# Kernel optimization log

Hardware: AMD Instinct MI355X
Metric: run time of the kernel (lower is better)

## Reference

```python
import jax, jax.numpy as jnp
import numpy as np

B, S, D = 16, 1024, 1024

def _xavier_uniform(key, shape, fan_in, fan_out):
    a = float(np.sqrt(6.0 / (fan_in + fan_out)))
    return jax.random.uniform(key, shape, jnp.float32, -a, a)

def setup_inputs() -> dict:
    key = jax.random.key(0)
    ks = jax.random.split(key, 8)
    query = jax.random.normal(ks[0], (B, S, D), jnp.float32)
    key_t = jax.random.normal(ks[1], (B, S, D), jnp.float32)
    value = jax.random.normal(ks[2], (B, S, D), jnp.float32)
    # learned additive attention bias [1, S, S], xavier_uniform init
    attn_bias = _xavier_uniform(ks[3], (1, S, S), S, S)
    # Linear weights (torch nn.Linear default: kaiming-uniform-ish; any init ok for baseline)
    Wq = _xavier_uniform(ks[4], (D, D), D, D)
    bq = jnp.zeros((D,), jnp.float32)
    Wk = _xavier_uniform(ks[5], (D, D), D, D)
    bk = jnp.zeros((D,), jnp.float32)
    return {"query": query, "key": key_t, "value": value,
            "attn_bias": attn_bias, "Wq": Wq, "bq": bq, "Wk": Wk, "bk": bk}

def reference(query, key, value, attn_bias, Wq, bq, Wk, bk):
    # q = query @ Wq^T + bq  (torch Linear convention)
    q = jnp.einsum('bsd,ed->bse', query, Wq) + bq            # [B,S,D]
    k = jnp.einsum('bsd,ed->bse', key, Wk) + bk              # [B,S,D]
    energy = jnp.einsum('bsd,btd->bst', q, k) + attn_bias    # [B,S,S] (bias broadcasts over B)
    attention = jax.nn.softmax(energy, axis=-1)
    out = jnp.einsum('bst,btd->bsd', attention, value)       # value is NOT projected (matches source)
    return (out, attention)
```

## Files before the change

### kernel.cpp

```cpp
#include <hip/hip_runtime.h>


#define AS1 __attribute__((address_space(1)))
#define AS3 __attribute__((address_space(3)))
#define VMCNT(n) asm volatile("s_waitcnt vmcnt(" #n ")" ::: "memory")
#define LGKM(n)  asm volatile("s_waitcnt lgkmcnt(" #n ")" ::: "memory")
#define SBARRIER asm volatile("s_barrier" ::: "memory")
#define SB0 __builtin_amdgcn_sched_barrier(0)

typedef __bf16 bf16;
typedef __bf16 bf16x4 __attribute__((ext_vector_type(4)));
typedef __bf16 bf16x8 __attribute__((ext_vector_type(8)));
typedef float  f32x4  __attribute__((ext_vector_type(4)));
typedef float  f32x16 __attribute__((ext_vector_type(16)));

constexpr int BATCH = 16;
constexpr int S = 1024;
constexpr int D = 1024;
constexpr long NBSD = (long)BATCH * S * D;

constexpr int GBM = 256, GBN = 256, GBK = 32;
constexpr int NTK = 1024 / GBK;
constexpr int ARR = GBM * GBK;

__device__ __forceinline__ void stage16(const bf16* src, const bf16* dst) {
  __builtin_amdgcn_global_load_lds((const AS1 void*)src, (AS3 void*)dst, 16, 0, 0);
}

__global__ __launch_bounds__(256) void split_convert(
    const float* __restrict__ in, bf16* __restrict__ hi, bf16* __restrict__ lo, int n4) {
  int i = blockIdx.x * blockDim.x + threadIdx.x;
  int stride = gridDim.x * blockDim.x;
  for (; i < n4; i += stride) {
    f32x4 x = ((const f32x4*)in)[i];
    bf16x4 h, l;
#pragma unroll
    for (int j = 0; j < 4; ++j) {
      float v = x[j];
      bf16 hh = (bf16)v;
      h[j] = hh;
      l[j] = (bf16)(v - (float)hh);
    }
    ((bf16x4*)hi)[i] = h;
    ((bf16x4*)lo)[i] = l;
  }
}

__global__ __launch_bounds__(256) void transpose_convert(
    const float* __restrict__ v, bf16* __restrict__ vT) {
  __shared__ float tile[32][33];
  const int b = blockIdx.z;
  const int t0 = blockIdx.y * 32, d0 = blockIdx.x * 32;
  const int tx = threadIdx.x & 31, ty = threadIdx.x >> 5;
  const float* src = v + (long)b * S * D;
#pragma unroll
  for (int i = 0; i < 4; ++i)
    tile[ty + i * 8][tx] = src[(long)(t0 + ty + i * 8) * D + d0 + tx];
  __syncthreads();
  bf16* dst = vT + (long)b * D * S;
#pragma unroll
  for (int i = 0; i < 4; ++i)
    dst[(long)(d0 + ty + i * 8) * S + t0 + tx] = (bf16)tile[tx][ty + i * 8];
}

template <int EPI>
__global__ __launch_bounds__(512, 2) void gemm32_split(
    const bf16* __restrict__ Ah_g, const bf16* __restrict__ Al_g, long a_bs,
    const bf16* __restrict__ Bh_g, const bf16* __restrict__ Bl_g, long b_bs,
    const float* __restrict__ bias,
    bf16* __restrict__ Ch, bf16* __restrict__ Cl,
    float* __restrict__ Cf, long c_bs) {
  __shared__ bf16 lds[2 * 4 * ARR];

  const int tid = threadIdx.x;
  const int lane = tid & 63, wid = tid >> 6;
  const int wr = wid >> 2, wc = wid & 3;
  const int lr = lane & 31;
  const int lk = lane >> 5;

  const int w = blockIdx.x;
  const int swz = (w & 7) * 32 + (w >> 3);
  int z, by, bx;
  if constexpr (EPI == 0) { z = 0; by = swz >> 2; bx = swz & 3; }
  else { z = swz >> 4; by = (swz >> 2) & 3; bx = swz & 3; }
  const long brow = (long)by * GBM, bcol = (long)bx * GBN;

  const bf16* A_h = Ah_g + (long)z * a_bs;
  const bf16* A_l = Al_g + (long)z * a_bs;
  const bf16* B_h = Bh_g + (long)z * b_bs;
  const bf16* B_l = Bl_g + (long)z * b_bs;

  const int srow = tid >> 2;
  const int csw = ((tid & 3) ^ ((srow >> 1) & 3)) * 8;
  const long asrc = (brow + srow) * 1024 + csw;
  const long bsrc = (bcol + srow) * 1024 + csw;
  const int dstoff = wid * 512;

  int aoff[4][2], boff[2][2];
#pragma unroll
  for (int i = 0; i < 4; ++i) {
    const int r = wr * 128 + i * 32 + lr;
#pragma unroll
    for (int s = 0; s < 2; ++s)
      aoff[i][s] = r * 32 + (((2 * s + lk) ^ ((r >> 1) & 3)) * 8);
  }
#pragma unroll
  for (int j = 0; j < 2; ++j) {
    const int r = wc * 64 + j * 32 + lr;
#pragma unroll
    for (int s = 0; s < 2; ++s)
      boff[j][s] = r * 32 + (((2 * s + lk) ^ ((r >> 1) & 3)) * 8);
  }

  f32x16 acc[4][2] = {};
  bf16x8 ahA[4][2], bhA[2][2], ahB[4][2], bhB[2][2], al[4][2], bl[2][2];

#define STG(slot, arr, base, koff, rr) \
  stage16((base) + (koff) + (long)(rr) * 131072, \
          lds + ((slot) * 4 + (arr)) * ARR + (rr) * 4096 + dstoff)

#define CLUSTER(AF, BF) \
  __builtin_amdgcn_s_setprio(1); \
  _Pragma("unroll") \
  for (int s = 0; s < 2; ++s) \
    _Pragma("unroll") \
    for (int i = 0; i < 4; ++i) \
      _Pragma("unroll") \
      for (int j = 0; j < 2; ++j) \
        acc[i][j] = __builtin_amdgcn_mfma_f32_32x32x16_bf16(AF[i][s], BF[j][s], acc[i][j], 0, 0, 0); \
  __builtin_amdgcn_s_setprio(0)

#define TILE_BODY(AH, BH, AHN, BHN, CUR, NXT, PF, KN) \
  { \
    const bf16* lA_l = lds + ((CUR) * 4 + 1) * ARR; \
    const bf16* lB_l = lds + ((CUR) * 4 + 3) * ARR; \
    const bf16* nA_h = lds + ((NXT) * 4 + 0) * ARR; \
    const bf16* nB_h = lds + ((NXT) * 4 + 2) * ARR; \
     \
    if (PF) { \
      STG(NXT, 0, A_h + asrc, KN, 0); STG(NXT, 0, A_h + asrc, KN, 1); \
      STG(NXT, 2, B_h + bsrc, KN, 0); STG(NXT, 2, B_h + bsrc, KN, 1); \
      VMCNT(6); \
    } else { VMCNT(2); } \
    SBARRIER; \
    _Pragma("unroll") \
    for (int j = 0; j < 2; ++j) \
      _Pragma("unroll") \
      for (int s = 0; s < 2; ++s) bl[j][s] = *(const bf16x8*)&lB_l[boff[j][s]]; \
    LGKM(4); SB0; \
    CLUSTER(AH, BH); \
     \
    if (PF) { STG(NXT, 3, B_l + bsrc, KN, 0); STG(NXT, 3, B_l + bsrc, KN, 1); VMCNT(6); } \
    else { VMCNT(0); } \
    SBARRIER; \
    _Pragma("unroll") \
    for (int i = 0; i < 4; ++i) \
      _Pragma("unroll") \
      for (int s = 0; s < 2; ++s) al[i][s] = *(const bf16x8*)&lA_l[aoff[i][s]]; \
    LGKM(8); SB0; \
    CLUSTER(AH, bl); \
     \
    if (PF) { STG(NXT, 1, A_l + asrc, KN, 0); STG(NXT, 1, A_l + asrc, KN, 1); VMCNT(4); } \
    SBARRIER; \
    if (PF) { \
      _Pragma("unroll") \
      for (int i = 0; i < 4; ++i) \
        _Pragma("unroll") \
        for (int s = 0; s < 2; ++s) AHN[i][s] = *(const bf16x8*)&nA_h[aoff[i][s]]; \
      _Pragma("unroll") \
      for (int j = 0; j < 2; ++j) \
        _Pragma("unroll") \
        for (int s = 0; s < 2; ++s) BHN[j][s] = *(const bf16x8*)&nB_h[boff[j][s]]; \
      LGKM(12); \
    } else { LGKM(0); } \
    SB0; \
    CLUSTER(al, BH); \
  }

  STG(0, 0, A_h + asrc, 0, 0); STG(0, 0, A_h + asrc, 0, 1);
  STG(0, 2, B_h + bsrc, 0, 0); STG(0, 2, B_h + bsrc, 0, 1);
  STG(0, 3, B_l + bsrc, 0, 0); STG(0, 3, B_l + bsrc, 0, 1);
  STG(0, 1, A_l + asrc, 0, 0); STG(0, 1, A_l + asrc, 0, 1);
  VMCNT(4);
  SBARRIER;
  {
    const bf16* lA_h0 = lds;
    const bf16* lB_h0 = lds + 2 * ARR;
#pragma unroll
    for (int i = 0; i < 4; ++i)
#pragma unroll
      for (int s = 0; s < 2; ++s) ahA[i][s] = *(const bf16x8*)&lA_h0[aoff[i][s]];
#pragma unroll
    for (int j = 0; j < 2; ++j)
#pragma unroll
      for (int s = 0; s < 2; ++s) bhA[j][s] = *(const bf16x8*)&lB_h0[boff[j][s]];
  }

  for (int tt = 0; tt < 15; ++tt) {
    const long k1 = (long)(2 * tt + 1) * GBK;
    const long k2 = (long)(2 * tt + 2) * GBK;
    TILE_BODY(ahA, bhA, ahB, bhB, 0, 1, true, k1);
    TILE_BODY(ahB, bhB, ahA, bhA, 1, 0, true, k2);
  }
  TILE_BODY(ahA, bhA, ahB, bhB, 0, 1, true, (long)31 * GBK);
  TILE_BODY(ahB, bhB, ahA, bhA, 1, 0, false, 0);
#undef STG
#undef CLUSTER
#undef TILE_BODY

  if constexpr (EPI == 0) {
#pragma unroll
    for (int j = 0; j < 2; ++j) {
      const long col = bcol + wc * 64 + j * 32 + lr;
      const float bv = bias[col];
#pragma unroll
      for (int i = 0; i < 4; ++i) {
        const long row0 = brow + wr * 128 + i * 32 + 4 * lk;
#pragma unroll
        for (int r = 0; r < 16; ++r) {
          const long row = row0 + (r & 3) + 8 * (r >> 2);
          const float c = acc[i][j][r] + bv;
          const bf16 h = (bf16)c;
          const bf16 l = (bf16)(c - (float)h);
          const long idx = row * 1024 + col;
          Ch[idx] = h;
          Cl[idx] = l;
        }
      }
    }
  } else {
    float* Cz = Cf + (long)z * c_bs;
#pragma unroll
    for (int j = 0; j < 2; ++j) {
      const long col = bcol + wc * 64 + j * 32 + lr;
#pragma unroll
      for (int i = 0; i < 4; ++i) {
        const long row0 = brow + wr * 128 + i * 32 + 4 * lk;
#pragma unroll
        for (int r = 0; r < 16; ++r) {
          const long row = row0 + (r & 3) + 8 * (r >> 2);
          Cz[row * 1024 + col] = acc[i][j][r] + bias[row * 1024 + col];
        }
      }
    }
  }
}

__global__ __launch_bounds__(512, 2) void gemm8_plain(
    const bf16* __restrict__ A_g, long a_bs,
    const bf16* __restrict__ B_g, long b_bs,
    float* __restrict__ C, long c_bs) {
  __shared__ bf16 lds[2 * 2 * ARR];

  const int tid = threadIdx.x;
  const int lane = tid & 63, wid = tid >> 6;
  const int wr = wid >> 2, wc = wid & 3;
  const int fr = lane & 15, fq = lane >> 4;
  const int fsw = (fr >> 1) & 3;

  const int w = blockIdx.x;
  const int swz = (w & 7) * 32 + (w >> 3);
  const int z = swz >> 4, by = (swz >> 2) & 3, bx = swz & 3;
  const long brow = (long)by * GBM, bcol = (long)bx * GBN;

  const bf16* A = A_g + (long)z * a_bs;
  const bf16* B = B_g + (long)z * b_bs;

  const int srow = tid >> 2;
  const int csw = ((tid & 3) ^ ((srow >> 1) & 3)) * 8;
  const long asrc = (brow + srow) * 1024 + csw;
  const long bsrc = (bcol + srow) * 1024 + csw;
  const int dstoff = wid * 512;

  const int aoffb = (wr * 128 + fr) * 32 + (fq ^ fsw) * 8;
  const int boffb = (wc * 64 + fr) * 32 + (fq ^ fsw) * 8;

  f32x4 acc[8][4] = {};

#define STG2(slot, arr, base, koff, rr) \
  stage16((base) + (koff) + (long)(rr) * 131072, \
          lds + ((slot) * 2 + (arr)) * ARR + (rr) * 4096 + dstoff)

  STG2(0, 0, A + asrc, 0, 0); STG2(0, 0, A + asrc, 0, 1);
  STG2(0, 1, B + bsrc, 0, 0); STG2(0, 1, B + bsrc, 0, 1);

  for (int t = 0; t < NTK; ++t) {
    const int cur = t & 1, nxt = cur ^ 1;
    const bf16* lA = lds + (cur * 2 + 0) * ARR;
    const bf16* lB = lds + (cur * 2 + 1) * ARR;

    if (t + 1 < NTK) {
      const long kn = (long)(t + 1) * GBK;
      STG2(nxt, 0, A + asrc, kn, 0); STG2(nxt, 0, A + asrc, kn, 1);
      STG2(nxt, 1, B + bsrc, kn, 0); STG2(nxt, 1, B + bsrc, kn, 1);
      VMCNT(4);
    } else {
      VMCNT(0);
    }
    SB0;
    SBARRIER;

    bf16x8 ah[8], bh[4];
#pragma unroll
    for (int m = 0; m < 8; ++m) ah[m] = *(const bf16x8*)&lA[aoffb + m * 512];
#pragma unroll
    for (int n = 0; n < 4; ++n) bh[n] = *(const bf16x8*)&lB[boffb + n * 512];
#pragma unroll
    for (int n = 0; n < 4; ++n)
#pragma unroll
      for (int m = 0; m < 8; ++m)
        acc[m][n] = __builtin_amdgcn_mfma_f32_16x16x32_bf16(ah[m], bh[n], acc[m][n], 0, 0, 0);

    SBARRIER;
  }
#undef STG2

  float* Cz = C + (long)z * c_bs;
#pragma unroll
  for (int n = 0; n < 4; ++n) {
    const long col = bcol + wc * 64 + n * 16 + fr;
#pragma unroll
    for (int m = 0; m < 8; ++m) {
      const long row0 = brow + wr * 128 + m * 16 + fq * 4;
#pragma unroll
      for (int j = 0; j < 4; ++j)
        Cz[(row0 + j) * 1024 + col] = acc[m][n][j];
    }
  }
}

__global__ __launch_bounds__(256) void softmax_rows(
    float* __restrict__ attn, bf16* __restrict__ attn_bf) {
  const long row = blockIdx.x;
  float* p = attn + row * 1024;
  const int tid = threadIdx.x, lane = tid & 63, wid = tid >> 6;

  f32x4 x = ((const f32x4*)p)[tid];
  float m = fmaxf(fmaxf(x[0], x[1]), fmaxf(x[2], x[3]));
#pragma unroll
  for (int off = 32; off; off >>= 1) m = fmaxf(m, __shfl_xor(m, off));
  __shared__ float redm[4];
  if (lane == 0) redm[wid] = m;
  __syncthreads();
  m = fmaxf(fmaxf(redm[0], redm[1]), fmaxf(redm[2], redm[3]));

  f32x4 e;
#pragma unroll
  for (int j = 0; j < 4; ++j) e[j] = __expf(x[j] - m);
  float s = e[0] + e[1] + e[2] + e[3];
#pragma unroll
  for (int off = 32; off; off >>= 1) s += __shfl_xor(s, off);
  __shared__ float reds[4];
  if (lane == 0) reds[wid] = s;
  __syncthreads();
  s = reds[0] + reds[1] + reds[2] + reds[3];

  const float inv = 1.0f / s;
  f32x4 r;
  bf16x4 rb;
#pragma unroll
  for (int j = 0; j < 4; ++j) {
    r[j] = e[j] * inv;
    rb[j] = (bf16)r[j];
  }
  ((f32x4*)p)[tid] = r;
  ((bf16x4*)(attn_bf + row * 1024))[tid] = rb;
}

extern "C" void kernel_launch(void* const* d_in, const int* in_sizes, int n_in,
                              void* d_out, int out_size, void* d_ws, size_t ws_size,
                              hipStream_t stream) {
  const float* query     = (const float*)d_in[0];
  const float* key       = (const float*)d_in[1];
  const float* value     = (const float*)d_in[2];
  const float* attn_bias = (const float*)d_in[3];
  const float* Wq        = (const float*)d_in[4];
  const float* bq        = (const float*)d_in[5];
  const float* Wk        = (const float*)d_in[6];
  const float* bk        = (const float*)d_in[7];

  float* out  = (float*)d_out;
  float* attn = out + NBSD;

  bf16* ws    = (bf16*)d_ws;
  bf16* q_hi  = ws;
  bf16* q_lo  = ws + NBSD;
  bf16* k_hi  = ws + 2 * NBSD;
  bf16* k_lo  = ws + 3 * NBSD;
  bf16* Wq_hi = ws + 4 * NBSD;
  bf16* Wq_lo = Wq_hi + (long)D * D;
  bf16* Wk_hi = Wq_lo + (long)D * D;
  bf16* Wk_lo = Wk_hi + (long)D * D;
  bf16* scr   = Wk_lo + (long)D * D;
  bf16* key_hi = scr;
  bf16* key_lo = scr + NBSD;
  bf16* valueT  = scr;
  bf16* attn_bf = scr + NBSD;
  bf16* query_hi = (bf16*)d_out;
  bf16* query_lo = query_hi + NBSD;

  split_convert<<<2048, 256, 0, stream>>>(query, query_hi, query_lo, (int)(NBSD / 4));
  split_convert<<<2048, 256, 0, stream>>>(key, key_hi, key_lo, (int)(NBSD / 4));
  split_convert<<<512, 256, 0, stream>>>(Wq, Wq_hi, Wq_lo, D * D / 4);
  split_convert<<<512, 256, 0, stream>>>(Wk, Wk_hi, Wk_lo, D * D / 4);

  gemm32_split<0><<<256, 512, 0, stream>>>(query_hi, query_lo, 0, Wq_hi, Wq_lo, 0,
                                           bq, q_hi, q_lo, nullptr, 0);
  gemm32_split<0><<<256, 512, 0, stream>>>(key_hi, key_lo, 0, Wk_hi, Wk_lo, 0,
                                           bk, k_hi, k_lo, nullptr, 0);

  transpose_convert<<<dim3(32, 32, 16), 256, 0, stream>>>(value, valueT);

  gemm32_split<1><<<256, 512, 0, stream>>>(q_hi, q_lo, (long)S * D, k_hi, k_lo, (long)S * D,
                                           attn_bias, nullptr, nullptr, attn, (long)S * S);

  softmax_rows<<<BATCH * S, 256, 0, stream>>>(attn, attn_bf);

  gemm8_plain<<<256, 512, 0, stream>>>(attn_bf, (long)S * S, valueT, (long)D * S,
                                       out, (long)S * D);
}
```

Baseline: 478.1 us.

## Fuse convert and projection launches, simplify split-GEMM pipeline, use 32x32 MFMA

Merges the four split_convert launches into one kernel and the two projection GEMMs into a single 512-block launch, so fewer kernels run back to back and each one fills the GPU better. The split-bf16 K loop drops the hand-interleaved double-register prefetch for a simpler loop that loads fragments and waits on lgkmcnt(0) before each MFMA cluster. This removes LDS/MFMA overlap inside a tile and adds barriers. The final plain GEMM moves from 16x16x32 to 32x32x16 MFMA with the same fragment layout as the split kernels.

```diff
diff --git a/kernel.cpp b/kernel.cpp
--- a/kernel.cpp
+++ b/kernel.cpp
@@ -27,10 +27,11 @@
   __builtin_amdgcn_global_load_lds((const AS1 void*)src, (AS3 void*)dst, 16, 0, 0);
 }
 
-__global__ __launch_bounds__(256) void split_convert(
-    const float* __restrict__ in, bf16* __restrict__ hi, bf16* __restrict__ lo, int n4) {
-  int i = blockIdx.x * blockDim.x + threadIdx.x;
-  int stride = gridDim.x * blockDim.x;
+__device__ __forceinline__ void conv_body(
+    const float* __restrict__ in, bf16* __restrict__ hi, bf16* __restrict__ lo,
+    int n4, int bid, int nb) {
+  int i = bid * 256 + threadIdx.x;
+  const int stride = nb * 256;
   for (; i < n4; i += stride) {
     f32x4 x = ((const f32x4*)in)[i];
     bf16x4 h, l;
@@ -46,6 +47,20 @@
   }
 }
 
+__global__ __launch_bounds__(256) void fused_converts(
+    const float* __restrict__ query, const float* __restrict__ key,
+    const float* __restrict__ Wq, const float* __restrict__ Wk,
+    bf16* __restrict__ q_hi, bf16* __restrict__ q_lo,
+    bf16* __restrict__ k_hi, bf16* __restrict__ k_lo,
+    bf16* __restrict__ Wq_hi, bf16* __restrict__ Wq_lo,
+    bf16* __restrict__ Wk_hi, bf16* __restrict__ Wk_lo) {
+  const int b = blockIdx.x;
+  if (b < 2048)       conv_body(query, q_hi, q_lo, (int)(NBSD / 4), b, 2048);
+  else if (b < 4096)  conv_body(key,  k_hi, k_lo, (int)(NBSD / 4), b - 2048, 2048);
+  else if (b < 4608)  conv_body(Wq, Wq_hi, Wq_lo, D * D / 4, b - 4096, 512);
+  else                conv_body(Wk, Wk_hi, Wk_lo, D * D / 4, b - 4608, 512);
+}
+
 __global__ __launch_bounds__(256) void transpose_convert(
     const float* __restrict__ v, bf16* __restrict__ vT) {
   __shared__ float tile[32][33];
@@ -63,14 +78,201 @@
     dst[(long)(d0 + ty + i * 8) * S + t0 + tx] = (bf16)tile[tx][ty + i * 8];
 }
 
-template <int EPI>
-__global__ __launch_bounds__(512, 2) void gemm32_split(
+#define STGM(slot, arr, base, koff, rr) \
+  stage16((base) + (koff) + (long)(rr) * 131072, \
+          lds + ((slot) * 4 + (arr)) * ARR + (rr) * 4096 + dstoff)
+
+#define CLUSTERM(AF, BF) \
+  __builtin_amdgcn_s_setprio(1); \
+  _Pragma("unroll") \
+  for (int s = 0; s < 2; ++s) \
+    _Pragma("unroll") \
+    for (int i = 0; i < 4; ++i) \
+      _Pragma("unroll") \
+      for (int j = 0; j < 2; ++j) \
+        acc[i][j] = __builtin_amdgcn_mfma_f32_32x32x16_bf16(AF[i][s], BF[j][s], acc[i][j], 0, 0, 0); \
+  __builtin_amdgcn_s_setprio(0)
+
+#define SPLIT_KLOOP \
+  STGM(0, 0, A_h + asrc, 0, 0); STGM(0, 0, A_h + asrc, 0, 1); \
+  STGM(0, 2, B_h + bsrc, 0, 0); STGM(0, 2, B_h + bsrc, 0, 1); \
+  STGM(0, 3, B_l + bsrc, 0, 0); STGM(0, 3, B_l + bsrc, 0, 1); \
+  STGM(0, 1, A_l + asrc, 0, 0); STGM(0, 1, A_l + asrc, 0, 1); \
+  VMCNT(4); \
+  SBARRIER; \
+  for (int t = 0; t < NTK; ++t) { \
+    const int cur = t & 1, nxt = cur ^ 1; \
+    const long kn = (long)(t + 1) * GBK; \
+    const bool pf = (t + 1 < NTK); \
+    const bf16* lA_h = lds + (cur * 4 + 0) * ARR; \
+    const bf16* lA_l = lds + (cur * 4 + 1) * ARR; \
+    const bf16* lB_h = lds + (cur * 4 + 2) * ARR; \
+    const bf16* lB_l = lds + (cur * 4 + 3) * ARR; \
+    _Pragma("unroll") \
+    for (int i = 0; i < 4; ++i) \
+      _Pragma("unroll") \
+      for (int s = 0; s < 2; ++s) ah[i][s] = *(const bf16x8*)&lA_h[aoff[i][s]]; \
+    _Pragma("unroll") \
+    for (int j = 0; j < 2; ++j) \
+      _Pragma("unroll") \
+      for (int s = 0; s < 2; ++s) bh[j][s] = *(const bf16x8*)&lB_h[boff[j][s]]; \
+    if (pf) { \
+      STGM(nxt, 0, A_h + asrc, kn, 0); STGM(nxt, 0, A_h + asrc, kn, 1); \
+      STGM(nxt, 2, B_h + bsrc, kn, 0); STGM(nxt, 2, B_h + bsrc, kn, 1); \
+      VMCNT(6); \
+    } else { VMCNT(2); } \
+    SBARRIER; LGKM(0); SB0; \
+    CLUSTERM(ah, bh); \
+    SBARRIER; \
+    _Pragma("unroll") \
+    for (int j = 0; j < 2; ++j) \
+      _Pragma("unroll") \
+      for (int s = 0; s < 2; ++s) bl[j][s] = *(const bf16x8*)&lB_l[boff[j][s]]; \
+    if (pf) { \
+      STGM(nxt, 3, B_l + bsrc, kn, 0); STGM(nxt, 3, B_l + bsrc, kn, 1); \
+      VMCNT(6); \
+    } else { VMCNT(0); } \
+    SBARRIER; LGKM(0); SB0; \
+    CLUSTERM(ah, bl); \
+    SBARRIER; \
+    _Pragma("unroll") \
+    for (int i = 0; i < 4; ++i) \
+      _Pragma("unroll") \
+      for (int s = 0; s < 2; ++s) al[i][s] = *(const bf16x8*)&lA_l[aoff[i][s]]; \
+    if (pf) { \
+      STGM(nxt, 1, A_l + asrc, kn, 0); STGM(nxt, 1, A_l + asrc, kn, 1); \
+      VMCNT(4); \
+    } \
+    SBARRIER; LGKM(0); SB0; \
+    CLUSTERM(al, bh); \
+    SBARRIER; \
+  }
+
+#define SPLIT_PREAMBLE \
+  const int tid = threadIdx.x; \
+  const int lane = tid & 63, wid = tid >> 6; \
+  const int wr = wid >> 2, wc = wid & 3; \
+  const int lr = lane & 31; \
+  const int lk = lane >> 5; \
+  const int srow = tid >> 2; \
+  const int csw = ((tid & 3) ^ ((srow >> 1) & 3)) * 8; \
+  const int dstoff = wid * 512; \
+  int aoff[4][2], boff[2][2]; \
+  _Pragma("unroll") \
+  for (int i = 0; i < 4; ++i) { \
+    const int r = wr * 128 + i * 32 + lr; \
+    _Pragma("unroll") \
+    for (int s = 0; s < 2; ++s) \
+      aoff[i][s] = r * 32 + (((2 * s + lk) ^ ((r >> 1) & 3)) * 8); \
+  } \
+  _Pragma("unroll") \
+  for (int j = 0; j < 2; ++j) { \
+    const int r = wc * 64 + j * 32 + lr; \
+    _Pragma("unroll") \
+    for (int s = 0; s < 2; ++s) \
+      boff[j][s] = r * 32 + (((2 * s + lk) ^ ((r >> 1) & 3)) * 8); \
+  } \
+  f32x16 acc[4][2] = {}; \
+  bf16x8 ah[4][2], al[4][2], bh[2][2], bl[2][2];
+
+__global__ __launch_bounds__(512, 2) void gemm32_proj2(
+    const bf16* __restrict__ qh, const bf16* __restrict__ ql,
+    const bf16* __restrict__ kh, const bf16* __restrict__ kl,
+    const bf16* __restrict__ Wqh, const bf16* __restrict__ Wql,
+    const bf16* __restrict__ Wkh, const bf16* __restrict__ Wkl,
+    const float* __restrict__ bq, const float* __restrict__ bk,
+    bf16* __restrict__ qoh, bf16* __restrict__ qol,
+    bf16* __restrict__ koh, bf16* __restrict__ kol) {
+  __shared__ bf16 lds[2 * 4 * ARR];
+
+  SPLIT_PREAMBLE
+
+  const int w = blockIdx.x;
+  const int swz = (w & 7) * 64 + (w >> 3);
+  const int op = swz >> 8;
+  const int rem = swz & 255;
+  const int by = rem >> 2, bx = rem & 3;
+  const long brow = (long)by * GBM, bcol = (long)bx * GBN;
+
+  const bf16* A_h = op ? kh : qh;
+  const bf16* A_l = op ? kl : ql;
+  const bf16* B_h = op ? Wkh : Wqh;
+  const bf16* B_l = op ? Wkl : Wql;
+  const float* bias = op ? bk : bq;
+  bf16* Ch = op ? koh : qoh;
+  bf16* Cl = op ? kol : qol;
+
+  const long asrc = (brow + srow) * 1024 + csw;
+  const long bsrc = (bcol + srow) * 1024 + csw;
+
+  SPLIT_KLOOP
+
+#pragma unroll
+  for (int j = 0; j < 2; ++j) {
+    const long col = bcol + wc * 64 + j * 32 + lr;
+    const float bv = bias[col];
+#pragma unroll
+    for (int i = 0; i < 4; ++i) {
+      const long row0 = brow + wr * 128 + i * 32 + 4 * lk;
+#pragma unroll
+      for (int r = 0; r < 16; ++r) {
+        const long row = row0 + (r & 3) + 8 * (r >> 2);
+        const float c = acc[i][j][r] + bv;
+        const bf16 h = (bf16)c;
+        const bf16 l = (bf16)(c - (float)h);
+        const long idx = row * 1024 + col;
+        Ch[idx] = h;
+        Cl[idx] = l;
+      }
+    }
+  }
+}
+
+__global__ __launch_bounds__(512, 2) void gemm32_energy(
     const bf16* __restrict__ Ah_g, const bf16* __restrict__ Al_g, long a_bs,
     const bf16* __restrict__ Bh_g, const bf16* __restrict__ Bl_g, long b_bs,
     const float* __restrict__ bias,
-    bf16* __restrict__ Ch, bf16* __restrict__ Cl,
     float* __restrict__ Cf, long c_bs) {
   __shared__ bf16 lds[2 * 4 * ARR];
+
+  SPLIT_PREAMBLE
+
+  const int w = blockIdx.x;
+  const int swz = (w & 7) * 32 + (w >> 3);
+  const int z = swz >> 4, by = (swz >> 2) & 3, bx = swz & 3;
+  const long brow = (long)by * GBM, bcol = (long)bx * GBN;
+
+  const bf16* A_h = Ah_g + (long)z * a_bs;
+  const bf16* A_l = Al_g + (long)z * a_bs;
+  const bf16* B_h = Bh_g + (long)z * b_bs;
+  const bf16* B_l = Bl_g + (long)z * b_bs;
+
+  const long asrc = (brow + srow) * 1024 + csw;
+  const long bsrc = (bcol + srow) * 1024 + csw;
+
+  SPLIT_KLOOP
+
+  float* Cz = Cf + (long)z * c_bs;
+#pragma unroll
+  for (int j = 0; j < 2; ++j) {
+    const long col = bcol + wc * 64 + j * 32 + lr;
+#pragma unroll
+    for (int i = 0; i < 4; ++i) {
+      const long row0 = brow + wr * 128 + i * 32 + 4 * lk;
+#pragma unroll
+      for (int r = 0; r < 16; ++r) {
+        const long row = row0 + (r & 3) + 8 * (r >> 2);
+        Cz[row * 1024 + col] = acc[i][j][r] + bias[row * 1024 + col];
+      }
+    }
+  }
+}
+
+__global__ __launch_bounds__(512, 2) void gemm32_plain(
+    const bf16* __restrict__ A_g, long a_bs,
+    const bf16* __restrict__ B_g, long b_bs,
+    float* __restrict__ C, long c_bs) {
+  __shared__ bf16 lds[2 * 2 * ARR];
 
   const int tid = threadIdx.x;
   const int lane = tid & 63, wid = tid >> 6;
@@ -80,15 +282,11 @@
 
   const int w = blockIdx.x;
   const int swz = (w & 7) * 32 + (w >> 3);
-  int z, by, bx;
-  if constexpr (EPI == 0) { z = 0; by = swz >> 2; bx = swz & 3; }
-  else { z = swz >> 4; by = (swz >> 2) & 3; bx = swz & 3; }
+  const int z = swz >> 4, by = (swz >> 2) & 3, bx = swz & 3;
   const long brow = (long)by * GBM, bcol = (long)bx * GBN;
 
-  const bf16* A_h = Ah_g + (long)z * a_bs;
-  const bf16* A_l = Al_g + (long)z * a_bs;
-  const bf16* B_h = Bh_g + (long)z * b_bs;
-  const bf16* B_l = Bl_g + (long)z * b_bs;
+  const bf16* A = A_g + (long)z * a_bs;
+  const bf16* B = B_g + (long)z * b_bs;
 
   const int srow = tid >> 2;
   const int csw = ((tid & 3) ^ ((srow >> 1) & 3)) * 8;
@@ -113,169 +311,7 @@
   }
 
   f32x16 acc[4][2] = {};
-  bf16x8 ahA[4][2], bhA[2][2], ahB[4][2], bhB[2][2], al[4][2], bl[2][2];
-
-#define STG(slot, arr, base, koff, rr) \
-  stage16((base) + (koff) + (long)(rr) * 131072, \
-          lds + ((slot) * 4 + (arr)) * ARR + (rr) * 4096 + dstoff)
-
-#define CLUSTER(AF, BF) \
-  __builtin_amdgcn_s_setprio(1); \
-  _Pragma("unroll") \
-  for (int s = 0; s < 2; ++s) \
-    _Pragma("unroll") \
-    for (int i = 0; i < 4; ++i) \
-      _Pragma("unroll") \
-      for (int j = 0; j < 2; ++j) \
-        acc[i][j] = __builtin_amdgcn_mfma_f32_32x32x16_bf16(AF[i][s], BF[j][s], acc[i][j], 0, 0, 0); \
-  __builtin_amdgcn_s_setprio(0)
-
-#define TILE_BODY(AH, BH, AHN, BHN, CUR, NXT, PF, KN) \
-  { \
-    const bf16* lA_l = lds + ((CUR) * 4 + 1) * ARR; \
-    const bf16* lB_l = lds + ((CUR) * 4 + 3) * ARR; \
-    const bf16* nA_h = lds + ((NXT) * 4 + 0) * ARR; \
-    const bf16* nB_h = lds + ((NXT) * 4 + 2) * ARR; \
-     \
-    if (PF) { \
-      STG(NXT, 0, A_h + asrc, KN, 0); STG(NXT, 0, A_h + asrc, KN, 1); \
-      STG(NXT, 2, B_h + bsrc, KN, 0); STG(NXT, 2, B_h + bsrc, KN, 1); \
-      VMCNT(6); \
-    } else { VMCNT(2); } \
-    SBARRIER; \
-    _Pragma("unroll") \
-    for (int j = 0; j < 2; ++j) \
-      _Pragma("unroll") \
-      for (int s = 0; s < 2; ++s) bl[j][s] = *(const bf16x8*)&lB_l[boff[j][s]]; \
-    LGKM(4); SB0; \
-    CLUSTER(AH, BH); \
-     \
-    if (PF) { STG(NXT, 3, B_l + bsrc, KN, 0); STG(NXT, 3, B_l + bsrc, KN, 1); VMCNT(6); } \
-    else { VMCNT(0); } \
-    SBARRIER; \
-    _Pragma("unroll") \
-    for (int i = 0; i < 4; ++i) \
-      _Pragma("unroll") \
-      for (int s = 0; s < 2; ++s) al[i][s] = *(const bf16x8*)&lA_l[aoff[i][s]]; \
-    LGKM(8); SB0; \
-    CLUSTER(AH, bl); \
-     \
-    if (PF) { STG(NXT, 1, A_l + asrc, KN, 0); STG(NXT, 1, A_l + asrc, KN, 1); VMCNT(4); } \
-    SBARRIER; \
-    if (PF) { \
-      _Pragma("unroll") \
-      for (int i = 0; i < 4; ++i) \
-        _Pragma("unroll") \
-        for (int s = 0; s < 2; ++s) AHN[i][s] = *(const bf16x8*)&nA_h[aoff[i][s]]; \
-      _Pragma("unroll") \
-      for (int j = 0; j < 2; ++j) \
-        _Pragma("unroll") \
-        for (int s = 0; s < 2; ++s) BHN[j][s] = *(const bf16x8*)&nB_h[boff[j][s]]; \
-      LGKM(12); \
-    } else { LGKM(0); } \
-    SB0; \
-    CLUSTER(al, BH); \
-  }
-
-  STG(0, 0, A_h + asrc, 0, 0); STG(0, 0, A_h + asrc, 0, 1);
-  STG(0, 2, B_h + bsrc, 0, 0); STG(0, 2, B_h + bsrc, 0, 1);
-  STG(0, 3, B_l + bsrc, 0, 0); STG(0, 3, B_l + bsrc, 0, 1);
-  STG(0, 1, A_l + asrc, 0, 0); STG(0, 1, A_l + asrc, 0, 1);
-  VMCNT(4);
-  SBARRIER;
-  {
-    const bf16* lA_h0 = lds;
-    const bf16* lB_h0 = lds + 2 * ARR;
-#pragma unroll
-    for (int i = 0; i < 4; ++i)
-#pragma unroll
-      for (int s = 0; s < 2; ++s) ahA[i][s] = *(const bf16x8*)&lA_h0[aoff[i][s]];
-#pragma unroll
-    for (int j = 0; j < 2; ++j)
-#pragma unroll
-      for (int s = 0; s < 2; ++s) bhA[j][s] = *(const bf16x8*)&lB_h0[boff[j][s]];
-  }
-
-  for (int tt = 0; tt < 15; ++tt) {
-    const long k1 = (long)(2 * tt + 1) * GBK;
-    const long k2 = (long)(2 * tt + 2) * GBK;
-    TILE_BODY(ahA, bhA, ahB, bhB, 0, 1, true, k1);
-    TILE_BODY(ahB, bhB, ahA, bhA, 1, 0, true, k2);
-  }
-  TILE_BODY(ahA, bhA, ahB, bhB, 0, 1, true, (long)31 * GBK);
-  TILE_BODY(ahB, bhB, ahA, bhA, 1, 0, false, 0);
-#undef STG
-#undef CLUSTER
-#undef TILE_BODY
-
-  if constexpr (EPI == 0) {
-#pragma unroll
-    for (int j = 0; j < 2; ++j) {
-      const long col = bcol + wc * 64 + j * 32 + lr;
-      const float bv = bias[col];
-#pragma unroll
-      for (int i = 0; i < 4; ++i) {
-        const long row0 = brow + wr * 128 + i * 32 + 4 * lk;
-#pragma unroll
-        for (int r = 0; r < 16; ++r) {
-          const long row = row0 + (r & 3) + 8 * (r >> 2);
-          const float c = acc[i][j][r] + bv;
-          const bf16 h = (bf16)c;
-          const bf16 l = (bf16)(c - (float)h);
-          const long idx = row * 1024 + col;
-          Ch[idx] = h;
-          Cl[idx] = l;
-        }
-      }
-    }
-  } else {
-    float* Cz = Cf + (long)z * c_bs;
-#pragma unroll
-    for (int j = 0; j < 2; ++j) {
-      const long col = bcol + wc * 64 + j * 32 + lr;
-#pragma unroll
-      for (int i = 0; i < 4; ++i) {
-        const long row0 = brow + wr * 128 + i * 32 + 4 * lk;
-#pragma unroll
-        for (int r = 0; r < 16; ++r) {
-          const long row = row0 + (r & 3) + 8 * (r >> 2);
-          Cz[row * 1024 + col] = acc[i][j][r] + bias[row * 1024 + col];
-        }
-      }
-    }
-  }
-}
-
-__global__ __launch_bounds__(512, 2) void gemm8_plain(
-    const bf16* __restrict__ A_g, long a_bs,
-    const bf16* __restrict__ B_g, long b_bs,
-    float* __restrict__ C, long c_bs) {
-  __shared__ bf16 lds[2 * 2 * ARR];
-
-  const int tid = threadIdx.x;
-  const int lane = tid & 63, wid = tid >> 6;
-  const int wr = wid >> 2, wc = wid & 3;
-  const int fr = lane & 15, fq = lane >> 4;
-  const int fsw = (fr >> 1) & 3;
-
-  const int w = blockIdx.x;
-  const int swz = (w & 7) * 32 + (w >> 3);
-  const int z = swz >> 4, by = (swz >> 2) & 3, bx = swz & 3;
-  const long brow = (long)by * GBM, bcol = (long)bx * GBN;
-
-  const bf16* A = A_g + (long)z * a_bs;
-  const bf16* B = B_g + (long)z * b_bs;
-
-  const int srow = tid >> 2;
-  const int csw = ((tid & 3) ^ ((srow >> 1) & 3)) * 8;
-  const long asrc = (brow + srow) * 1024 + csw;
-  const long bsrc = (bcol + srow) * 1024 + csw;
-  const int dstoff = wid * 512;
-
-  const int aoffb = (wr * 128 + fr) * 32 + (fq ^ fsw) * 8;
-  const int boffb = (wc * 64 + fr) * 32 + (fq ^ fsw) * 8;
-
-  f32x4 acc[8][4] = {};
+  bf16x8 af[4][2], bf_[2][2];
 
 #define STG2(slot, arr, base, koff, rr) \
   stage16((base) + (koff) + (long)(rr) * 131072, \
@@ -300,16 +336,24 @@
     SB0;
     SBARRIER;
 
-    bf16x8 ah[8], bh[4];
-#pragma unroll
-    for (int m = 0; m < 8; ++m) ah[m] = *(const bf16x8*)&lA[aoffb + m * 512];
-#pragma unroll
-    for (int n = 0; n < 4; ++n) bh[n] = *(const bf16x8*)&lB[boffb + n * 512];
-#pragma unroll
-    for (int n = 0; n < 4; ++n)
-#pragma unroll
-      for (int m = 0; m < 8; ++m)
-        acc[m][n] = __builtin_amdgcn_mfma_f32_16x16x32_bf16(ah[m], bh[n], acc[m][n], 0, 0, 0);
+#pragma unroll
+    for (int i = 0; i < 4; ++i)
+#pragma unroll
+      for (int s = 0; s < 2; ++s) af[i][s] = *(const bf16x8*)&lA[aoff[i][s]];
+#pragma unroll
+    for (int j = 0; j < 2; ++j)
+#pragma unroll
+      for (int s = 0; s < 2; ++s) bf_[j][s] = *(const bf16x8*)&lB[boff[j][s]];
+    LGKM(0); SB0;
+    __builtin_amdgcn_s_setprio(1);
+#pragma unroll
+    for (int s = 0; s < 2; ++s)
+#pragma unroll
+      for (int i = 0; i < 4; ++i)
+#pragma unroll
+        for (int j = 0; j < 2; ++j)
+          acc[i][j] = __builtin_amdgcn_mfma_f32_32x32x16_bf16(af[i][s], bf_[j][s], acc[i][j], 0, 0, 0);
+    __builtin_amdgcn_s_setprio(0);
 
     SBARRIER;
   }
@@ -317,14 +361,16 @@
 
   float* Cz = C + (long)z * c_bs;
 #pragma unroll
-  for (int n = 0; n < 4; ++n) {
-    const long col = bcol + wc * 64 + n * 16 + fr;
-#pragma unroll
-    for (int m = 0; m < 8; ++m) {
-      const long row0 = brow + wr * 128 + m * 16 + fq * 4;
-#pragma unroll
-      for (int j = 0; j < 4; ++j)
-        Cz[(row0 + j) * 1024 + col] = acc[m][n][j];
+  for (int j = 0; j < 2; ++j) {
+    const long col = bcol + wc * 64 + j * 32 + lr;
+#pragma unroll
+    for (int i = 0; i < 4; ++i) {
+      const long row0 = brow + wr * 128 + i * 32 + 4 * lk;
+#pragma unroll
+      for (int r = 0; r < 16; ++r) {
+        const long row = row0 + (r & 3) + 8 * (r >> 2);
+        Cz[row * 1024 + col] = acc[i][j][r];
+      }
     }
   }
 }
@@ -399,23 +445,22 @@
   bf16* query_hi = (bf16*)d_out;
   bf16* query_lo = query_hi + NBSD;
 
-  split_convert<<<2048, 256, 0, stream>>>(query, query_hi, query_lo, (int)(NBSD / 4));
-  split_convert<<<2048, 256, 0, stream>>>(key, key_hi, key_lo, (int)(NBSD / 4));
-  split_convert<<<512, 256, 0, stream>>>(Wq, Wq_hi, Wq_lo, D * D / 4);
-  split_convert<<<512, 256, 0, stream>>>(Wk, Wk_hi, Wk_lo, D * D / 4);
-
-  gemm32_split<0><<<256, 512, 0, stream>>>(query_hi, query_lo, 0, Wq_hi, Wq_lo, 0,
-                                           bq, q_hi, q_lo, nullptr, 0);
-  gemm32_split<0><<<256, 512, 0, stream>>>(key_hi, key_lo, 0, Wk_hi, Wk_lo, 0,
-                                           bk, k_hi, k_lo, nullptr, 0);
+  fused_converts<<<5120, 256, 0, stream>>>(query, key, Wq, Wk,
+                                           query_hi, query_lo, key_hi, key_lo,
+                                           Wq_hi, Wq_lo, Wk_hi, Wk_lo);
+
+  gemm32_proj2<<<512, 512, 0, stream>>>(query_hi, query_lo, key_hi, key_lo,
+                                        Wq_hi, Wq_lo, Wk_hi, Wk_lo,
+                                        bq, bk,
+                                        q_hi, q_lo, k_hi, k_lo);
 
   transpose_convert<<<dim3(32, 32, 16), 256, 0, stream>>>(value, valueT);
 
-  gemm32_split<1><<<256, 512, 0, stream>>>(q_hi, q_lo, (long)S * D, k_hi, k_lo, (long)S * D,
-                                           attn_bias, nullptr, nullptr, attn, (long)S * S);
+  gemm32_energy<<<256, 512, 0, stream>>>(q_hi, q_lo, (long)S * D, k_hi, k_lo, (long)S * D,
+                                         attn_bias, attn, (long)S * S);
 
   softmax_rows<<<BATCH * S, 256, 0, stream>>>(attn, attn_bf);
 
-  gemm8_plain<<<256, 512, 0, stream>>>(attn_bf, (long)S * S, valueT, (long)D * S,
-                                       out, (long)S * D);
-}
+  gemm32_plain<<<256, 512, 0, stream>>>(attn_bf, (long)S * S, valueT, (long)D * S,
+                                        out, (long)S * D);
+}
```

After: 424.3 us (median of 2 runs). 11.3% less time.
